# Performance work log

Hardware: AMD Instinct MI355X
Metric: run time of the kernel (lower is better)

## Reference

```python
import jax, jax.numpy as jnp
import numpy as np

N, D, H, T = 50000, 512, 512, 16
N_HOP = 1
NEG = -1e18


def setup_inputs() -> dict:
    key = jax.random.key(0)
    ks = jax.random.split(key, 16)
    s = 0.05  # param init scale
    inp = {
        "attn_mem": jax.random.normal(ks[0], (N, D), jnp.float32),
        "stop": jax.random.uniform(ks[1], (D,), jnp.float32, -0.01, 0.01),
        "init_h": jax.random.normal(ks[2], (H,), jnp.float32) * s,
        "init_c": jax.random.normal(ks[3], (H,), jnp.float32) * s,
        "init_i": jax.random.normal(ks[4], (D,), jnp.float32) * s,
        "attn_wm": jax.random.normal(ks[5], (D, H), jnp.float32) * s,
        "attn_wq": jax.random.normal(ks[6], (H, H), jnp.float32) * s,
        "attn_v": jax.random.normal(ks[7], (H,), jnp.float32) * s,
        "hop_wm": jax.random.normal(ks[8], (D, H), jnp.float32) * s,
        "hop_wq": jax.random.normal(ks[9], (H, H), jnp.float32) * s,
        "hop_v": jax.random.normal(ks[10], (H,), jnp.float32) * s,
        "w_ih": jax.random.normal(ks[11], (4 * H, D), jnp.float32) * s,
        "w_hh": jax.random.normal(ks[12], (4 * H, H), jnp.float32) * s,
        "b_ih": jax.random.normal(ks[13], (4 * H,), jnp.float32) * s,
        "b_hh": jax.random.normal(ks[14], (4 * H,), jnp.float32) * s,
        # precomputed gumbel noise -> categorical sampling via gumbel-max
        "gumbel": jax.random.gumbel(ks[15], (T, N + 1), jnp.float32),
    }
    return inp


def _attn_score(feat, q, v, w):
    # feat: [M, H], q: [H] -> unnormalized scores [M]
    return jnp.tanh(feat + q @ w) @ v


def reference(attn_mem, stop, init_h, init_c, init_i, attn_wm, attn_wq, attn_v,
              hop_wm, hop_wq, hop_v, w_ih, w_hh, b_ih, b_hh, gumbel):
    mem = jnp.concatenate([attn_mem, stop[None, :]], axis=0)  # [N+1, D]
    attn_feat = mem @ attn_wm                                  # [N+1, H]
    hop_feat = mem @ hop_wm                                    # [N+1, H]
    stop_idx = mem.shape[0] - 1

    def lstm_cell(x, h, c):
        gates = x @ w_ih.T + b_ih + h @ w_hh.T + b_hh          # [4H]
        i, f, g, o = jnp.split(gates, 4)
        i, f, o = jax.nn.sigmoid(i), jax.nn.sigmoid(f), jax.nn.sigmoid(o)
        c_new = f * c + i * jnp.tanh(g)
        return o * jnp.tanh(c_new), c_new

    def step(carry, g):
        h, c, x, sel, done = carry
        h, c = lstm_cell(x, h, c)
        q = h
        for _ in range(N_HOP):  # glimpse hops
            s = _attn_score(hop_feat, q, hop_v, hop_wq)
            q = jax.nn.softmax(s) @ hop_feat
        score = _attn_score(attn_feat, q, attn_v, attn_wq)     # [N+1]
        score = jnp.where(sel, NEG, score)                     # mask selected
        logp_all = jax.nn.log_softmax(score)
        out = jnp.argmax(score + g)                            # Categorical sample
        logp = jnp.where(done, 0.0, logp_all[out])
        out_rec = jnp.where(done, stop_idx, out)
        sel = jnp.where(done, sel, sel.at[out].set(True))
        new_done = done | (out == stop_idx)
        x = jnp.where(new_done, x, mem[out])
        return (h, c, x, sel, new_done), (out_rec.astype(jnp.int32), logp)

    carry0 = (init_h, init_c, init_i,
              jnp.zeros((mem.shape[0],), jnp.bool_), jnp.array(False))
    _, (outs, logps) = jax.lax.scan(step, carry0, gumbel)
    return outs, logps
```

## Files before the change

kernel.cpp:

```cpp
#include <hip/hip_runtime.h>
#include <math.h>

#define NITEMS 50000
#define NROWS 50001
#define NP 50176
#define DD 512
#define HH 512
#define TT 16
#define NEGV (-1e18f)
#define NGRP 784
#define NGC 196

typedef unsigned long long ull;
typedef unsigned short ushort;
typedef short short8 __attribute__((ext_vector_type(8)));
typedef float f32x4 __attribute__((ext_vector_type(4)));

#define AST(p, v) __hip_atomic_store((p), (v), __ATOMIC_RELAXED, __HIP_MEMORY_SCOPE_AGENT)
#define ALD(p) __hip_atomic_load((p), __ATOMIC_RELAXED, __HIP_MEMORY_SCOPE_AGENT)
#define AADD_REL(p) __hip_atomic_fetch_add((p), 1u, __ATOMIC_ACQ_REL, __HIP_MEMORY_SCOPE_AGENT)
#define FLAG_SET(p) __hip_atomic_store((p), 1u, __ATOMIC_RELEASE, __HIP_MEMORY_SCOPE_AGENT)
#define FLAG_GET(p) __hip_atomic_load((p), __ATOMIC_ACQUIRE, __HIP_MEMORY_SCOPE_AGENT)

__device__ __forceinline__ unsigned fkey(float f) {
  unsigned u = __float_as_uint(f);
  return (u & 0x80000000u) ? ~u : (u | 0x80000000u);
}
__device__ __forceinline__ float ftanh(float x) {
  float e = __builtin_amdgcn_exp2f(x * 2.885390081777927f);
  return 1.f - 2.f * __builtin_amdgcn_rcpf(e + 1.f);
}
__device__ __forceinline__ float fexp(float x) {
  return __builtin_amdgcn_exp2f(x * 1.4426950408889634f);
}
__device__ __forceinline__ ushort rne1(float a) {
  unsigned u = __float_as_uint(a);
  return (ushort)((u + 0x7fffu + ((u >> 16) & 1u)) >> 16);
}
__device__ __forceinline__ float bf2f(ushort h) { return __uint_as_float((unsigned)h << 16); }
__device__ __forceinline__ unsigned pack_bf16(float a, float b) {
  return (unsigned)rne1(a) | ((unsigned)rne1(b) << 16);
}
__device__ __forceinline__ float bflo(unsigned u) { return __uint_as_float(u << 16); }
__device__ __forceinline__ float bfhi(unsigned u) { return __uint_as_float(u & 0xffff0000u); }

__device__ __forceinline__ void gl_lds16(const void* g, void* l) {
#if __has_builtin(__builtin_amdgcn_global_load_lds)
  __builtin_amdgcn_global_load_lds((const __attribute__((address_space(1))) unsigned*)g,
                                   (__attribute__((address_space(3))) unsigned*)l, 16, 0, 0);
#else
  const int lane = threadIdx.x & 63;
  *(uint4*)((char*)l + lane * 16) = *(const uint4*)g;
#endif
}

#define MFMA(a, b, c) __builtin_amdgcn_mfma_f32_16x16x32_bf16(a, b, c, 0, 0, 0)

__global__ void k_convA(const float* __restrict__ A0, const float* __restrict__ stoprow,
                        ushort* __restrict__ Ahi, ushort* __restrict__ Alo) {
  const size_t t = (size_t)blockIdx.x * 256 + threadIdx.x;
  const size_t base = t * 8;
  const int row = (int)(base >> 9);
  float v[8];
  if (row < NITEMS) {
    const float4* p = (const float4*)(A0 + base);
    float4 x = p[0], y = p[1];
    v[0] = x.x; v[1] = x.y; v[2] = x.z; v[3] = x.w;
    v[4] = y.x; v[5] = y.y; v[6] = y.z; v[7] = y.w;
  } else if (row == NITEMS) {
    const float4* p = (const float4*)(stoprow + (base & 511));
    float4 x = p[0], y = p[1];
    v[0] = x.x; v[1] = x.y; v[2] = x.z; v[3] = x.w;
    v[4] = y.x; v[5] = y.y; v[6] = y.z; v[7] = y.w;
  } else {
#pragma unroll
    for (int j = 0; j < 8; ++j) v[j] = 0.f;
  }
  unsigned hw[4], lw[4];
#pragma unroll
  for (int j = 0; j < 4; ++j) {
    float a0 = v[2 * j], a1 = v[2 * j + 1];
    ushort h0 = rne1(a0), h1 = rne1(a1);
    hw[j] = (unsigned)h0 | ((unsigned)h1 << 16);
    lw[j] = pack_bf16(a0 - bf2f(h0), a1 - bf2f(h1));
  }
  *(uint4*)(Ahi + base) = make_uint4(hw[0], hw[1], hw[2], hw[3]);
  *(uint4*)(Alo + base) = make_uint4(lw[0], lw[1], lw[2], lw[3]);
}

__global__ void k_convBT(const float* __restrict__ W, ushort* __restrict__ WhiT,
                         ushort* __restrict__ WloT) {
  const int n = blockIdx.x;
  const int k0 = threadIdx.x * 2;
  float a0 = W[(size_t)k0 * 512 + n];
  float a1 = W[(size_t)(k0 + 1) * 512 + n];
  ushort h0 = rne1(a0), h1 = rne1(a1);
  *(unsigned*)(WhiT + (size_t)n * 512 + k0) = (unsigned)h0 | ((unsigned)h1 << 16);
  *(unsigned*)(WloT + (size_t)n * 512 + k0) = pack_bf16(a0 - bf2f(h0), a1 - bf2f(h1));
}

template <int TR>
__launch_bounds__(256, 2)
__global__ void k_mfma(const ushort* __restrict__ Ahi, const ushort* __restrict__ Alo,
                       const ushort* __restrict__ BhT, const ushort* __restrict__ BlT,
                       ushort* __restrict__ C) {
  __shared__ __align__(16) char lds[65536];
  char* sA0 = lds;
  char* sA1 = lds + 16384;
  char* sB0 = lds + 32768;
  char* sB1 = lds + 49152;
  const int tid = threadIdx.x;
  const int lane = tid & 63, w = tid >> 6;
  const int lid = blockIdx.y * 4 + blockIdx.x;
  const int xcd = lid & 7, pos = lid >> 3;
  const int orig = xcd * 196 + pos;
  const int m0 = (orig >> 2) * 128, n0 = (orig & 3) * 128;
  const int aR0 = (w & 1) * 64, bR0 = (w >> 1) * 64;

  f32x4 acc[4][4];
  const f32x4 z4 = {0.f, 0.f, 0.f, 0.f};
#pragma unroll
  for (int i = 0; i < 4; ++i)
#pragma unroll
    for (int j = 0; j < 4; ++j) acc[i][j] = z4;

#define STAGE_ALL(KT)                                                                     \
  {                                                                                       \
    _Pragma("unroll") for (int i = 0; i < 4; ++i) {                                       \
      const int row = i * 32 + (tid >> 3);                                                \
      const int kb = ((tid & 7) << 4) ^ ((row & 7) << 4);                                 \
      const int ldso = i * 4096 + (w << 10);                                              \
      gl_lds16((const char*)(Ahi + ((size_t)(m0 + row) << 9) + (KT)) + kb, sA0 + ldso);   \
      gl_lds16((const char*)(Alo + ((size_t)(m0 + row) << 9) + (KT)) + kb, sA1 + ldso);   \
      gl_lds16((const char*)(BhT + ((size_t)(n0 + row) << 9) + (KT)) + kb, sB0 + ldso);   \
      gl_lds16((const char*)(BlT + ((size_t)(n0 + row) << 9) + (KT)) + kb, sB1 + ldso);   \
    }                                                                                     \
  }

  STAGE_ALL(0)
  __syncthreads();
  for (int c = 0; c < 8; ++c) {
#pragma unroll
    for (int ks = 0; ks < 2; ++ks) {
      short8 ah[4], al[4], bh[4], bl[4];
      const int kbb = ks * 64 + ((lane >> 4) << 4);
#pragma unroll
      for (int f = 0; f < 4; ++f) {
        const int ra = aR0 + f * 16 + (lane & 15);
        const int oa = ra * 128 + (kbb ^ ((ra & 7) << 4));
        ah[f] = *(const short8*)(sA0 + oa);
        al[f] = *(const short8*)(sA1 + oa);
        const int rb = bR0 + f * 16 + (lane & 15);
        const int ob = rb * 128 + (kbb ^ ((rb & 7) << 4));
        bh[f] = *(const short8*)(sB0 + ob);
        bl[f] = *(const short8*)(sB1 + ob);
      }
#pragma unroll
      for (int mf = 0; mf < 4; ++mf)
#pragma unroll
        for (int nf = 0; nf < 4; ++nf) {
          acc[mf][nf] = MFMA(ah[mf], bh[nf], acc[mf][nf]);
          acc[mf][nf] = MFMA(ah[mf], bl[nf], acc[mf][nf]);
          acc[mf][nf] = MFMA(al[mf], bh[nf], acc[mf][nf]);
        }
    }
    if (c < 7) {
      __syncthreads();
      STAGE_ALL((c + 1) * 64)
      __syncthreads();
    }
  }
#undef STAGE_ALL

#pragma unroll
  for (int mf = 0; mf < 4; ++mf)
#pragma unroll
    for (int nf = 0; nf < 4; ++nf) {
      const f32x4 a = acc[mf][nf];
      const int n = n0 + bR0 + nf * 16 + (lane & 15);
      const int mb = m0 + aR0 + mf * 16 + ((lane >> 4) << 2);
      if (TR) {
        ushort* p = C + (size_t)n * NP + mb;
        *(uint2*)p = make_uint2(pack_bf16(a.x, a.y), pack_bf16(a.z, a.w));
      } else {
        C[(size_t)(mb + 0) * 512 + n] = rne1(a.x);
        C[(size_t)(mb + 1) * 512 + n] = rne1(a.y);
        C[(size_t)(mb + 2) * 512 + n] = rne1(a.z);
        C[(size_t)(mb + 3) * 512 + n] = rne1(a.w);
      }
    }
}

__global__ void k_zero(int* __restrict__ sel, unsigned* __restrict__ cnts) {
  int i = blockIdx.x * 256 + threadIdx.x;
  if (i < NROWS) sel[i] = 0;
  if (blockIdx.x == 0 && threadIdx.x < 80) cnts[threadIdx.x] = 0;
}

__launch_bounds__(256)
__global__ void k_A(const float* __restrict__ attn_mem, const float* __restrict__ stoprow,
                    const float* __restrict__ init_i, const float* __restrict__ init_h,
                    const float* __restrict__ init_c,
                    const float* __restrict__ w_ih, const float* __restrict__ w_hh,
                    const float* __restrict__ b_ih, const float* __restrict__ b_hh,
                    const float* __restrict__ hop_wq,
                    float* __restrict__ hv0, float* __restrict__ hv1,
                    float* __restrict__ cv0, float* __restrict__ cv1,
                    float* __restrict__ b1, const int* __restrict__ xrow_buf,
                    unsigned* __restrict__ cntA, unsigned* __restrict__ flagA, int t) {
  __shared__ float g4[4];
  __shared__ float hs[512];
  __shared__ float red2[256];
  __shared__ int sOld;
  const int b = blockIdx.x, tid = threadIdx.x, w = tid >> 6, lane = tid & 63;
  const int xrow = (t == 0) ? -1 : *xrow_buf;
  const float* xp = (xrow < 0) ? init_i
                               : ((xrow == NITEMS) ? stoprow : attn_mem + (size_t)xrow * DD);
  const float* hsrc = (t == 0) ? init_h : ((t & 1) ? hv0 : hv1);
  float* hdst = (t & 1) ? hv1 : hv0;
  const float* csrc = (t == 0) ? init_c : ((t & 1) ? cv0 : cv1);
  float* cdst = (t & 1) ? cv1 : cv0;

  const int r = w * 512 + b;
  const float4* x4 = (const float4*)xp;
  const float4* h4 = (const float4*)hsrc;
  const float4* wi = (const float4*)(w_ih + (size_t)r * DD);
  const float4* wh = (const float4*)(w_hh + (size_t)r * DD);
  float s = 0.f;
  float4 a, ww;
  a = x4[lane * 2];     ww = wi[lane * 2];     s += a.x * ww.x + a.y * ww.y + a.z * ww.z + a.w * ww.w;
  a = x4[lane * 2 + 1]; ww = wi[lane * 2 + 1]; s += a.x * ww.x + a.y * ww.y + a.z * ww.z + a.w * ww.w;
  a = h4[lane * 2];     ww = wh[lane * 2];     s += a.x * ww.x + a.y * ww.y + a.z * ww.z + a.w * ww.w;
  a = h4[lane * 2 + 1]; ww = wh[lane * 2 + 1]; s += a.x * ww.x + a.y * ww.y + a.z * ww.z + a.w * ww.w;
#pragma unroll
  for (int off = 32; off > 0; off >>= 1) s += __shfl_xor(s, off);
  if (lane == 0) g4[w] = s + b_ih[r] + b_hh[r];
  __syncthreads();
  if (tid == 0) {
    const float si = 1.f / (1.f + expf(-g4[0]));
    const float sf = 1.f / (1.f + expf(-g4[1]));
    const float so = 1.f / (1.f + expf(-g4[3]));
    const float cn = sf * csrc[b] + si * tanhf(g4[2]);
    cdst[b] = cn;
    AST(&hdst[b], so * tanhf(cn));
  }
  __syncthreads();
  if (tid == 0) {
    unsigned old = AADD_REL(cntA);
    if (old == 511u) { FLAG_SET(flagA); AST(cntA, 0u); }
    sOld = (int)old;
  }
  __syncthreads();
  const int old = sOld;
  if (old >= 496) {
    if (tid == 0 && old != 511) {
      while (FLAG_GET(flagA) == 0u) {}
    }
    __syncthreads();
    const int c0 = (old - 496) * 32;
    hs[tid] = ALD(&hdst[tid]);
    hs[tid + 256] = ALD(&hdst[tid + 256]);
    __syncthreads();
    const int col = c0 + (tid & 31), seg = tid >> 5;
    float acc = 0.f;
#pragma unroll 8
    for (int i = seg * 64; i < seg * 64 + 64; ++i)
      acc = fmaf(hs[i], hop_wq[(size_t)i * 512 + col], acc);
    red2[tid] = acc;
    __syncthreads();
    if (tid < 32) {
      float sm = 0.f;
#pragma unroll
      for (int g2 = 0; g2 < 8; ++g2) sm += red2[tid + 32 * g2];
      b1[c0 + tid] = sm;
    }
  }
}

__launch_bounds__(512)
__global__ void k_B1(const ushort* __restrict__ featT, const float* __restrict__ b1v,
                     const float* __restrict__ hv, float* __restrict__ e,
                     float* __restrict__ bZ1, float* __restrict__ Zt,
                     unsigned* __restrict__ cntB1) {
  __shared__ float spart[8][256];
  __shared__ float rz[512];
  __shared__ int isLast;
  const int tid = threadIdx.x, g = blockIdx.x;
  const int w = tid >> 6, lane = tid & 63;
  const int mb = g * 256 + lane * 4;
  const int h0 = w * 64;
  const ushort* fp = featT + (size_t)h0 * NP + mb;
  float a0 = 0.f, a1 = 0.f, a2 = 0.f, a3 = 0.f;
#pragma unroll 8
  for (int hh = 0; hh < 64; ++hh) {
    const uint2 u = *(const uint2*)fp;
    fp += NP;
    const float bb = b1v[h0 + hh], vv = hv[h0 + hh];
    a0 += ftanh(bflo(u.x) + bb) * vv;
    a1 += ftanh(bfhi(u.x) + bb) * vv;
    a2 += ftanh(bflo(u.y) + bb) * vv;
    a3 += ftanh(bfhi(u.y) + bb) * vv;
  }
  spart[w][lane * 4 + 0] = a0;
  spart[w][lane * 4 + 1] = a1;
  spart[w][lane * 4 + 2] = a2;
  spart[w][lane * 4 + 3] = a3;
  __syncthreads();
  if (w < 4) {
    const int idx = w * 64 + lane;
    const int m = g * 256 + idx;
    float s = 0.f;
#pragma unroll
    for (int w2 = 0; w2 < 8; ++w2) s += spart[w2][idx];
    float ev = (m < NROWS) ? fexp(s) : 0.f;
    e[m] = ev;
    float Z = ev;
#pragma unroll
    for (int off = 32; off > 0; off >>= 1) Z += __shfl_xor(Z, off);
    if (lane == 0) AST(&bZ1[g * 4 + w], Z);
  }
  __syncthreads();
  if (tid == 0) {
    unsigned old = AADD_REL(cntB1);
    isLast = (old == gridDim.x - 1);
    if (isLast) AST(cntB1, 0u);
  }
  __syncthreads();
  if (isLast) {
    float Zl = 0.f;
    for (int i = tid; i < NGRP; i += 512) Zl += ALD(&bZ1[i]);
    rz[tid] = Zl;
    __syncthreads();
    for (int s2 = 256; s2 > 0; s2 >>= 1) {
      if (tid < s2) rz[tid] += rz[tid + s2];
      __syncthreads();
    }
    if (tid == 0) *Zt = rz[0];
  }
}

__launch_bounds__(256)
__global__ void k_B2(const ushort* __restrict__ featT, const float* __restrict__ e,
                     const float* __restrict__ Zt, const float* __restrict__ attn_wq,
                     float* __restrict__ qn, float* __restrict__ b2,
                     unsigned* __restrict__ cntB2, unsigned* __restrict__ flagB2) {
  __shared__ float red[256];
  __shared__ int sOld;
  const int tid = threadIdx.x, h = blockIdx.x;
  const ushort* fr = featT + (size_t)h * NP;
  float acc = 0.f;
#pragma unroll 4
  for (int m0 = tid * 8; m0 < NP; m0 += 2048) {
    const uint4 F = *(const uint4*)(fr + m0);
    const float4 e0 = *(const float4*)(e + m0);
    const float4 e1 = *(const float4*)(e + m0 + 4);
    acc += bflo(F.x) * e0.x + bfhi(F.x) * e0.y + bflo(F.y) * e0.z + bfhi(F.y) * e0.w +
           bflo(F.z) * e1.x + bfhi(F.z) * e1.y + bflo(F.w) * e1.z + bfhi(F.w) * e1.w;
  }
  red[tid] = acc;
  __syncthreads();
  for (int s2 = 128; s2 > 0; s2 >>= 1) {
    if (tid < s2) red[tid] += red[tid + s2];
    __syncthreads();
  }
  if (tid == 0) AST(&qn[h], red[0] / (*Zt));
  __syncthreads();
  if (tid == 0) {
    unsigned old = AADD_REL(cntB2);
    if (old == 511u) { FLAG_SET(flagB2); AST(cntB2, 0u); }
    sOld = (int)old;
  }
  __syncthreads();
  const int old = sOld;
  if (old >= 504) {
    const int li = old - 504;
    if (tid == 0 && old != 511) {
      while (FLAG_GET(flagB2) == 0u) {}
    }
    __syncthreads();
    const int j = li * 64 + (tid & 63), is = tid >> 6;
    float a = 0.f;
#pragma unroll 8
    for (int i2 = is * 128; i2 < is * 128 + 128; ++i2)
      a = fmaf(ALD(&qn[i2]), attn_wq[(size_t)i2 * 512 + j], a);
    red[tid] = a;
    __syncthreads();
    if (tid < 64) b2[li * 64 + tid] = red[tid] + red[tid + 64] + red[tid + 128] + red[tid + 192];
  }
}

__launch_bounds__(512)
__global__ void k_C(const ushort* __restrict__ featT, const float* __restrict__ b2,
                    const float* __restrict__ av, int* __restrict__ sel,
                    const float* __restrict__ gum,
                    float* __restrict__ bZa, ull* __restrict__ bkey, float* __restrict__ bsc,
                    int* __restrict__ done_buf, int* __restrict__ xrow_buf,
                    float* __restrict__ outf, unsigned* __restrict__ cntC, int t) {
  __shared__ float spart[8][256];
  __shared__ float rz[512];
  __shared__ ull rk[512];
  __shared__ float rs[512];
  __shared__ int isLast;
  const int tid = threadIdx.x, g = blockIdx.x;
  const int w = tid >> 6, lane = tid & 63;
  const int mb = g * 256 + lane * 4;
  const int h0 = w * 64;
  const ushort* fp = featT + (size_t)h0 * NP + mb;
  float a0 = 0.f, a1 = 0.f, a2 = 0.f, a3 = 0.f;
#pragma unroll 8
  for (int hh = 0; hh < 64; ++hh) {
    const uint2 u = *(const uint2*)fp;
    fp += NP;
    const float bb = b2[h0 + hh], vv = av[h0 + hh];
    a0 += ftanh(bflo(u.x) + bb) * vv;
    a1 += ftanh(bfhi(u.x) + bb) * vv;
    a2 += ftanh(bflo(u.y) + bb) * vv;
    a3 += ftanh(bfhi(u.y) + bb) * vv;
  }
  spart[w][lane * 4 + 0] = a0;
  spart[w][lane * 4 + 1] = a1;
  spart[w][lane * 4 + 2] = a2;
  spart[w][lane * 4 + 3] = a3;
  __syncthreads();
  if (w < 4) {
    const int idx = w * 64 + lane;
    const int m = g * 256 + idx;
    float s = 0.f;
#pragma unroll
    for (int w2 = 0; w2 < 8; ++w2) s += spart[w2][idx];
    const bool valid = (m < NROWS);
    float Z, sv;
    ull key;
    if (valid) {
      const float se = sel[m] ? NEGV : s;
      sv = se;
      key = ((ull)fkey(se + gum[m]) << 32) | (unsigned)(NITEMS - m);
      Z = fexp(se);
    } else {
      key = 0;
      Z = 0.f;
      sv = 0.f;
    }
#pragma unroll
    for (int off = 32; off > 0; off >>= 1) {
      Z += __shfl_xor(Z, off);
      ull Ko = __shfl_xor(key, off);
      float so = __shfl_xor(sv, off);
      if (Ko > key) { key = Ko; sv = so; }
    }
    if (lane == 0) {
      AST(&bZa[g * 4 + w], Z);
      AST(&bkey[g * 4 + w], key);
      AST(&bsc[g * 4 + w], sv);
    }
  }
  __syncthreads();
  if (tid == 0) {
    unsigned old = AADD_REL(cntC);
    isLast = (old == gridDim.x - 1);
    if (isLast) AST(cntC, 0u);
  }
  __syncthreads();
  if (isLast) {
    float Zl = 0.f, Sl = 0.f;
    ull Kl = 0;
    for (int i = tid; i < NGRP; i += 512) {
      Zl += ALD(&bZa[i]);
      ull k = ALD(&bkey[i]);
      if (k > Kl) { Kl = k; Sl = ALD(&bsc[i]); }
    }
    rz[tid] = Zl;
    rk[tid] = Kl;
    rs[tid] = Sl;
    __syncthreads();
    for (int s2 = 256; s2 > 0; s2 >>= 1) {
      if (tid < s2) {
        rz[tid] += rz[tid + s2];
        if (rk[tid + s2] > rk[tid]) { rk[tid] = rk[tid + s2]; rs[tid] = rs[tid + s2]; }
      }
      __syncthreads();
    }
    if (tid == 0) {
      const float Z = rz[0];
      const ull K = rk[0];
      const int out = NITEMS - (int)(unsigned)(K & 0xffffffffull);
      const int d_in = (t == 0) ? 0 : *done_buf;
      const int xprev = (t == 0) ? -1 : *xrow_buf;
      const int nd = d_in | (out == NITEMS);
      outf[t] = (float)(d_in ? NITEMS : out);
      outf[TT + t] = d_in ? 0.f : (rs[0] - logf(Z));
      if (!d_in) sel[out] = 1;
      *done_buf = nd;
      *xrow_buf = nd ? xprev : out;
    }
  }
}

extern "C" void kernel_launch(void* const* d_in, const int* in_sizes, int n_in,
                              void* d_out, int out_size, void* d_ws, size_t ws_size,
                              hipStream_t stream) {
  const float* attn_mem = (const float*)d_in[0];
  const float* stoprow  = (const float*)d_in[1];
  const float* init_h   = (const float*)d_in[2];
  const float* init_c   = (const float*)d_in[3];
  const float* init_i   = (const float*)d_in[4];
  const float* attn_wm  = (const float*)d_in[5];
  const float* attn_wq  = (const float*)d_in[6];
  const float* attn_v   = (const float*)d_in[7];
  const float* hop_wm   = (const float*)d_in[8];
  const float* hop_wq   = (const float*)d_in[9];
  const float* hop_v    = (const float*)d_in[10];
  const float* w_ih     = (const float*)d_in[11];
  const float* w_hh     = (const float*)d_in[12];
  const float* b_ih     = (const float*)d_in[13];
  const float* b_hh     = (const float*)d_in[14];
  const float* gumbel   = (const float*)d_in[15];

  float* ws = (float*)d_ws;
  size_t fo = 0;
  const size_t FB = (size_t)NP * 512 / 2;
  ushort* hop_featT  = (ushort*)(ws + fo); fo += FB;
  ushort* attn_featT = (ushort*)(ws + fo); fo += FB;
  ushort* Ahi = (ushort*)(ws + fo); fo += FB;
  ushort* Alo = (ushort*)(ws + fo); fo += FB;
  ushort* WhiT_a = (ushort*)(ws + fo); fo += 131072;
  ushort* WloT_a = (ushort*)(ws + fo); fo += 131072;
  ushort* WhiT_h = (ushort*)(ws + fo); fo += 131072;
  ushort* WloT_h = (ushort*)(ws + fo); fo += 131072;
  int* sel   = (int*)(ws + fo); fo += NP;
  float* e   = ws + fo; fo += NP;
  float* bZ1 = ws + fo; fo += 1024;
  float* bZa = ws + fo; fo += 1024;
  float* bsc = ws + fo; fo += 1024;
  ull* bkey  = (ull*)(ws + fo); fo += 2048;
  float* hv0 = ws + fo; fo += HH;
  float* hv1 = ws + fo; fo += HH;
  float* cv0 = ws + fo; fo += HH;
  float* cv1 = ws + fo; fo += HH;
  float* b1  = ws + fo; fo += HH;
  float* b2  = ws + fo; fo += HH;
  float* qn  = ws + fo; fo += HH;
  float* Ztp = ws + fo; fo += 2;
  unsigned* cnts = (unsigned*)(ws + fo); fo += 80;
  int* done_buf = (int*)(ws + fo); fo += 2;
  int* xrow_buf = (int*)(ws + fo); fo += 2;
  if (fo * sizeof(float) > ws_size) return;

  float* outf = (float*)d_out;

  k_zero<<<NP / 256, 256, 0, stream>>>(sel, cnts);
  k_convA<<<(NP * 512 / 8) / 256, 256, 0, stream>>>(attn_mem, stoprow, Ahi, Alo);
  k_convBT<<<512, 256, 0, stream>>>(attn_wm, WhiT_a, WloT_a);
  k_convBT<<<512, 256, 0, stream>>>(hop_wm, WhiT_h, WloT_h);

  dim3 ggrid(4, NP / 128);
  k_mfma<1><<<ggrid, 256, 0, stream>>>(Ahi, Alo, WhiT_a, WloT_a, attn_featT);
  k_mfma<1><<<ggrid, 256, 0, stream>>>(Ahi, Alo, WhiT_h, WloT_h, hop_featT);

  for (int t = 0; t < TT; ++t) {
    k_A<<<512, 256, 0, stream>>>(attn_mem, stoprow, init_i, init_h, init_c,
                                 w_ih, w_hh, b_ih, b_hh, hop_wq,
                                 hv0, hv1, cv0, cv1, b1, xrow_buf,
                                 cnts + 0, cnts + 16 + t, t);
    k_B1<<<NGC, 512, 0, stream>>>(hop_featT, b1, hop_v, e, bZ1, Ztp, cnts + 1);
    k_B2<<<512, 256, 0, stream>>>(hop_featT, e, Ztp, attn_wq, qn, b2,
                                  cnts + 3, cnts + 32 + t);
    k_C<<<NGC, 512, 0, stream>>>(attn_featT, b2, attn_v, sel,
                                 gumbel + (size_t)t * NROWS, bZa, bkey, bsc,
                                 done_buf, xrow_buf, outf, cnts + 2, t);
  }
}
```

Before: 1.624 ms.

## Fuse per-step kernels into one grid-synchronized step kernel

```diff
diff --git a/kernel.cpp b/kernel.cpp
--- a/kernel.cpp
+++ b/kernel.cpp
@@ -9,7 +9,7 @@
 #define TT 16
 #define NEGV (-1e18f)
 #define NGRP 784
-#define NGC 196
+#define NSB 512
 
 typedef unsigned long long ull;
 typedef unsigned short ushort;
@@ -99,7 +99,6 @@
   *(unsigned*)(WloT + (size_t)n * 512 + k0) = pack_bf16(a0 - bf2f(h0), a1 - bf2f(h1));
 }
 
-template <int TR>
 __launch_bounds__(256, 2)
 __global__ void k_mfma(const ushort* __restrict__ Ahi, const ushort* __restrict__ Alo,
                        const ushort* __restrict__ BhT, const ushort* __restrict__ BlT,
@@ -179,22 +178,15 @@
       const f32x4 a = acc[mf][nf];
       const int n = n0 + bR0 + nf * 16 + (lane & 15);
       const int mb = m0 + aR0 + mf * 16 + ((lane >> 4) << 2);
-      if (TR) {
-        ushort* p = C + (size_t)n * NP + mb;
-        *(uint2*)p = make_uint2(pack_bf16(a.x, a.y), pack_bf16(a.z, a.w));
-      } else {
-        C[(size_t)(mb + 0) * 512 + n] = rne1(a.x);
-        C[(size_t)(mb + 1) * 512 + n] = rne1(a.y);
-        C[(size_t)(mb + 2) * 512 + n] = rne1(a.z);
-        C[(size_t)(mb + 3) * 512 + n] = rne1(a.w);
-      }
+      ushort* p = C + (size_t)n * NP + mb;
+      *(uint2*)p = make_uint2(pack_bf16(a.x, a.y), pack_bf16(a.z, a.w));
     }
 }
 
 __global__ void k_zero(int* __restrict__ sel, unsigned* __restrict__ cnts) {
   int i = blockIdx.x * 256 + threadIdx.x;
   if (i < NROWS) sel[i] = 0;
-  if (blockIdx.x == 0 && threadIdx.x < 80) cnts[threadIdx.x] = 0;
+  if (blockIdx.x == 0 && threadIdx.x < 128) cnts[threadIdx.x] = 0;
 }
 
 __launch_bounds__(256)
@@ -213,7 +205,7 @@
   __shared__ float red2[256];
   __shared__ int sOld;
   const int b = blockIdx.x, tid = threadIdx.x, w = tid >> 6, lane = tid & 63;
-  const int xrow = (t == 0) ? -1 : *xrow_buf;
+  const int xrow = (t == 0) ? -1 : ALD((int*)xrow_buf);
   const float* xp = (xrow < 0) ? init_i
                                : ((xrow == NITEMS) ? stoprow : attn_mem + (size_t)xrow * DD);
   const float* hsrc = (t == 0) ? init_h : ((t & 1) ? hv0 : hv1);
@@ -254,7 +246,7 @@
   const int old = sOld;
   if (old >= 496) {
     if (tid == 0 && old != 511) {
-      while (FLAG_GET(flagA) == 0u) {}
+      while (FLAG_GET(flagA) == 0u) __builtin_amdgcn_s_sleep(2);
     }
     __syncthreads();
     const int c0 = (old - 496) * 32;
@@ -277,221 +269,316 @@
   }
 }
 
-__launch_bounds__(512)
-__global__ void k_B1(const ushort* __restrict__ featT, const float* __restrict__ b1v,
-                     const float* __restrict__ hv, float* __restrict__ e,
-                     float* __restrict__ bZ1, float* __restrict__ Zt,
-                     unsigned* __restrict__ cntB1) {
-  __shared__ float spart[8][256];
-  __shared__ float rz[512];
-  __shared__ int isLast;
-  const int tid = threadIdx.x, g = blockIdx.x;
+struct SP {
+  const ushort *hopT, *attnT;
+  const float *b1v, *hop_v, *attn_wq, *attn_v, *gumbel;
+  float *e, *bZ1, *qn, *b2, *bZa, *bsc;
+  ull* bkey;
+  int* sel;
+  int *done_buf, *xrow_buf;
+  float* outf;
+  const float *attn_mem, *stoprow, *init_i, *init_h, *init_c;
+  const float *w_ih, *w_hh, *b_ih, *b_hh, *hop_wq;
+  float *hv0, *hv1, *cv0, *cv1, *b1out;
+  unsigned* cnts;
+  int t;
+};
+
+union SMu {
+  struct { float spart[4][128]; float bias[512]; float vv[512]; } sw;
+  struct { float red[256]; } r;
+  struct { float rz[256]; ull rk[256]; float rs[256]; } fin;
+  struct { float g4[4]; float hs[512]; float red2[256]; } pa;
+};
+
+__launch_bounds__(256)
+__global__ void k_step(SP p) {
+  __shared__ SMu sm;
+  __shared__ int sOld;
+  const int tid = threadIdx.x, b = blockIdx.x;
   const int w = tid >> 6, lane = tid & 63;
-  const int mb = g * 256 + lane * 4;
-  const int h0 = w * 64;
-  const ushort* fp = featT + (size_t)h0 * NP + mb;
-  float a0 = 0.f, a1 = 0.f, a2 = 0.f, a3 = 0.f;
+  const int t = p.t;
+  unsigned* c1 = p.cnts + 0;
+  unsigned* c2 = p.cnts + 1;
+  unsigned* c2b = p.cnts + 2;
+  unsigned* c3 = p.cnts + 3;
+  unsigned* cA = p.cnts + 4;
+  unsigned* f1 = p.cnts + 16 + t;
+  unsigned* f2a = p.cnts + 32 + t;
+  unsigned* f2 = p.cnts + 48 + t;
+  unsigned* fF = p.cnts + 64 + t;
+  unsigned* fA = p.cnts + 80 + t;
+
+  for (int i = tid; i < 512; i += 256) {
+    sm.sw.bias[i] = p.b1v[i];
+    sm.sw.vv[i] = p.hop_v[i];
+  }
+  __syncthreads();
+  if (b < 392) {
+    const int mb = b * 128 + lane * 2;
+    const int h0 = w * 128;
+    const ushort* fp = p.hopT + (size_t)h0 * NP + mb;
+    float a0 = 0.f, a1 = 0.f;
 #pragma unroll 8
-  for (int hh = 0; hh < 64; ++hh) {
-    const uint2 u = *(const uint2*)fp;
-    fp += NP;
-    const float bb = b1v[h0 + hh], vv = hv[h0 + hh];
-    a0 += ftanh(bflo(u.x) + bb) * vv;
-    a1 += ftanh(bfhi(u.x) + bb) * vv;
-    a2 += ftanh(bflo(u.y) + bb) * vv;
-    a3 += ftanh(bfhi(u.y) + bb) * vv;
-  }
-  spart[w][lane * 4 + 0] = a0;
-  spart[w][lane * 4 + 1] = a1;
-  spart[w][lane * 4 + 2] = a2;
-  spart[w][lane * 4 + 3] = a3;
-  __syncthreads();
-  if (w < 4) {
-    const int idx = w * 64 + lane;
-    const int m = g * 256 + idx;
-    float s = 0.f;
-#pragma unroll
-    for (int w2 = 0; w2 < 8; ++w2) s += spart[w2][idx];
-    float ev = (m < NROWS) ? fexp(s) : 0.f;
-    e[m] = ev;
-    float Z = ev;
-#pragma unroll
-    for (int off = 32; off > 0; off >>= 1) Z += __shfl_xor(Z, off);
-    if (lane == 0) AST(&bZ1[g * 4 + w], Z);
+    for (int hh = 0; hh < 128; ++hh) {
+      const unsigned u = *(const unsigned*)fp;
+      fp += NP;
+      const float bb = sm.sw.bias[h0 + hh], vv = sm.sw.vv[h0 + hh];
+      a0 += ftanh(bflo(u) + bb) * vv;
+      a1 += ftanh(bfhi(u) + bb) * vv;
+    }
+    sm.sw.spart[w][lane * 2] = a0;
+    sm.sw.spart[w][lane * 2 + 1] = a1;
+    __syncthreads();
+    if (w < 2) {
+      const int idx = w * 64 + lane;
+      const int m = b * 128 + idx;
+      float s = sm.sw.spart[0][idx] + sm.sw.spart[1][idx] + sm.sw.spart[2][idx] +
+                sm.sw.spart[3][idx];
+      float ev = (m < NROWS) ? fexp(s) : 0.f;
+      p.e[m] = ev;
+      float Z = ev;
+#pragma unroll
+      for (int off = 32; off > 0; off >>= 1) Z += __shfl_xor(Z, off);
+      if (lane == 0) AST(&p.bZ1[b * 2 + w], Z);
+    }
   }
   __syncthreads();
   if (tid == 0) {
-    unsigned old = AADD_REL(cntB1);
-    isLast = (old == gridDim.x - 1);
-    if (isLast) AST(cntB1, 0u);
-  }
-  __syncthreads();
-  if (isLast) {
-    float Zl = 0.f;
-    for (int i = tid; i < NGRP; i += 512) Zl += ALD(&bZ1[i]);
-    rz[tid] = Zl;
-    __syncthreads();
-    for (int s2 = 256; s2 > 0; s2 >>= 1) {
-      if (tid < s2) rz[tid] += rz[tid + s2];
-      __syncthreads();
-    }
-    if (tid == 0) *Zt = rz[0];
-  }
-}
-
-__launch_bounds__(256)
-__global__ void k_B2(const ushort* __restrict__ featT, const float* __restrict__ e,
-                     const float* __restrict__ Zt, const float* __restrict__ attn_wq,
-                     float* __restrict__ qn, float* __restrict__ b2,
-                     unsigned* __restrict__ cntB2, unsigned* __restrict__ flagB2) {
-  __shared__ float red[256];
-  __shared__ int sOld;
-  const int tid = threadIdx.x, h = blockIdx.x;
-  const ushort* fr = featT + (size_t)h * NP;
-  float acc = 0.f;
+    unsigned old = AADD_REL(c1);
+    if (old == NSB - 1u) { FLAG_SET(f1); AST(c1, 0u); }
+    else { while (FLAG_GET(f1) == 0u) __builtin_amdgcn_s_sleep(2); }
+  }
+  __syncthreads();
+
+  {
+    const ushort* fr = p.hopT + (size_t)b * NP;
+    float acc = 0.f;
 #pragma unroll 4
-  for (int m0 = tid * 8; m0 < NP; m0 += 2048) {
-    const uint4 F = *(const uint4*)(fr + m0);
-    const float4 e0 = *(const float4*)(e + m0);
-    const float4 e1 = *(const float4*)(e + m0 + 4);
-    acc += bflo(F.x) * e0.x + bfhi(F.x) * e0.y + bflo(F.y) * e0.z + bfhi(F.y) * e0.w +
-           bflo(F.z) * e1.x + bfhi(F.z) * e1.y + bflo(F.w) * e1.z + bfhi(F.w) * e1.w;
-  }
-  red[tid] = acc;
-  __syncthreads();
-  for (int s2 = 128; s2 > 0; s2 >>= 1) {
-    if (tid < s2) red[tid] += red[tid + s2];
-    __syncthreads();
-  }
-  if (tid == 0) AST(&qn[h], red[0] / (*Zt));
+    for (int m0 = tid * 8; m0 < NP; m0 += 2048) {
+      const uint4 F = *(const uint4*)(fr + m0);
+      const float4 e0 = *(const float4*)(p.e + m0);
+      const float4 e1 = *(const float4*)(p.e + m0 + 4);
+      acc += bflo(F.x) * e0.x + bfhi(F.x) * e0.y + bflo(F.y) * e0.z + bfhi(F.y) * e0.w +
+             bflo(F.z) * e1.x + bfhi(F.z) * e1.y + bflo(F.w) * e1.z + bfhi(F.w) * e1.w;
+    }
+    sm.r.red[tid] = acc;
+    __syncthreads();
+    for (int s2 = 128; s2 > 0; s2 >>= 1) {
+      if (tid < s2) sm.r.red[tid] += sm.r.red[tid + s2];
+      __syncthreads();
+    }
+    if (tid == 0) AST(&p.qn[b], sm.r.red[0]);
+  }
   __syncthreads();
   if (tid == 0) {
-    unsigned old = AADD_REL(cntB2);
-    if (old == 511u) { FLAG_SET(flagB2); AST(cntB2, 0u); }
+    unsigned old = AADD_REL(c2);
     sOld = (int)old;
-  }
-  __syncthreads();
-  const int old = sOld;
-  if (old >= 504) {
-    const int li = old - 504;
-    if (tid == 0 && old != 511) {
-      while (FLAG_GET(flagB2) == 0u) {}
-    }
-    __syncthreads();
+    if (old == NSB - 1u) { FLAG_SET(f2a); AST(c2, 0u); }
+    else if (old >= NSB - 8u) {
+      while (FLAG_GET(f2a) == 0u) __builtin_amdgcn_s_sleep(2);
+    }
+  }
+  __syncthreads();
+  const int o2 = sOld;
+  if (o2 >= NSB - 8) {
+    float zl = 0.f;
+    for (int i = tid; i < NGRP; i += 256) zl += ALD(&p.bZ1[i]);
+    sm.r.red[tid] = zl;
+    __syncthreads();
+    for (int s2 = 128; s2 > 0; s2 >>= 1) {
+      if (tid < s2) sm.r.red[tid] += sm.r.red[tid + s2];
+      __syncthreads();
+    }
+    const float Zt = sm.r.red[0];
+    __syncthreads();
+    const int li = o2 - (NSB - 8);
     const int j = li * 64 + (tid & 63), is = tid >> 6;
     float a = 0.f;
 #pragma unroll 8
     for (int i2 = is * 128; i2 < is * 128 + 128; ++i2)
-      a = fmaf(ALD(&qn[i2]), attn_wq[(size_t)i2 * 512 + j], a);
-    red[tid] = a;
-    __syncthreads();
-    if (tid < 64) b2[li * 64 + tid] = red[tid] + red[tid + 64] + red[tid + 128] + red[tid + 192];
-  }
-}
-
-__launch_bounds__(512)
-__global__ void k_C(const ushort* __restrict__ featT, const float* __restrict__ b2,
-                    const float* __restrict__ av, int* __restrict__ sel,
-                    const float* __restrict__ gum,
-                    float* __restrict__ bZa, ull* __restrict__ bkey, float* __restrict__ bsc,
-                    int* __restrict__ done_buf, int* __restrict__ xrow_buf,
-                    float* __restrict__ outf, unsigned* __restrict__ cntC, int t) {
-  __shared__ float spart[8][256];
-  __shared__ float rz[512];
-  __shared__ ull rk[512];
-  __shared__ float rs[512];
-  __shared__ int isLast;
-  const int tid = threadIdx.x, g = blockIdx.x;
-  const int w = tid >> 6, lane = tid & 63;
-  const int mb = g * 256 + lane * 4;
-  const int h0 = w * 64;
-  const ushort* fp = featT + (size_t)h0 * NP + mb;
-  float a0 = 0.f, a1 = 0.f, a2 = 0.f, a3 = 0.f;
+      a = fmaf(ALD(&p.qn[i2]), p.attn_wq[(size_t)i2 * 512 + j], a);
+    sm.r.red[tid] = a;
+    __syncthreads();
+    if (tid < 64)
+      AST(&p.b2[li * 64 + tid],
+          (sm.r.red[tid] + sm.r.red[tid + 64] + sm.r.red[tid + 128] + sm.r.red[tid + 192]) / Zt);
+    __syncthreads();
+    if (tid == 0) {
+      unsigned ob = AADD_REL(c2b);
+      if (ob == 7u) { FLAG_SET(f2); AST(c2b, 0u); }
+    }
+  }
+  if (tid == 0) {
+    while (FLAG_GET(f2) == 0u) __builtin_amdgcn_s_sleep(2);
+  }
+  __syncthreads();
+
+  for (int i = tid; i < 512; i += 256) {
+    sm.sw.bias[i] = ALD(&p.b2[i]);
+    sm.sw.vv[i] = p.attn_v[i];
+  }
+  __syncthreads();
+  if (b < 392) {
+    const int mb = b * 128 + lane * 2;
+    const int h0 = w * 128;
+    const ushort* fp = p.attnT + (size_t)h0 * NP + mb;
+    float a0 = 0.f, a1 = 0.f;
 #pragma unroll 8
-  for (int hh = 0; hh < 64; ++hh) {
-    const uint2 u = *(const uint2*)fp;
-    fp += NP;
-    const float bb = b2[h0 + hh], vv = av[h0 + hh];
-    a0 += ftanh(bflo(u.x) + bb) * vv;
-    a1 += ftanh(bfhi(u.x) + bb) * vv;
-    a2 += ftanh(bflo(u.y) + bb) * vv;
-    a3 += ftanh(bfhi(u.y) + bb) * vv;
-  }
-  spart[w][lane * 4 + 0] = a0;
-  spart[w][lane * 4 + 1] = a1;
-  spart[w][lane * 4 + 2] = a2;
-  spart[w][lane * 4 + 3] = a3;
-  __syncthreads();
-  if (w < 4) {
-    const int idx = w * 64 + lane;
-    const int m = g * 256 + idx;
-    float s = 0.f;
-#pragma unroll
-    for (int w2 = 0; w2 < 8; ++w2) s += spart[w2][idx];
-    const bool valid = (m < NROWS);
-    float Z, sv;
-    ull key;
-    if (valid) {
-      const float se = sel[m] ? NEGV : s;
-      sv = se;
-      key = ((ull)fkey(se + gum[m]) << 32) | (unsigned)(NITEMS - m);
-      Z = fexp(se);
-    } else {
-      key = 0;
-      Z = 0.f;
-      sv = 0.f;
-    }
-#pragma unroll
-    for (int off = 32; off > 0; off >>= 1) {
-      Z += __shfl_xor(Z, off);
-      ull Ko = __shfl_xor(key, off);
-      float so = __shfl_xor(sv, off);
-      if (Ko > key) { key = Ko; sv = so; }
-    }
-    if (lane == 0) {
-      AST(&bZa[g * 4 + w], Z);
-      AST(&bkey[g * 4 + w], key);
-      AST(&bsc[g * 4 + w], sv);
+    for (int hh = 0; hh < 128; ++hh) {
+      const unsigned u = *(const unsigned*)fp;
+      fp += NP;
+      const float bb = sm.sw.bias[h0 + hh], vv = sm.sw.vv[h0 + hh];
+      a0 += ftanh(bflo(u) + bb) * vv;
+      a1 += ftanh(bfhi(u) + bb) * vv;
+    }
+    sm.sw.spart[w][lane * 2] = a0;
+    sm.sw.spart[w][lane * 2 + 1] = a1;
+    __syncthreads();
+    if (w < 2) {
+      const int idx = w * 64 + lane;
+      const int m = b * 128 + idx;
+      float s = sm.sw.spart[0][idx] + sm.sw.spart[1][idx] + sm.sw.spart[2][idx] +
+                sm.sw.spart[3][idx];
+      const bool valid = (m < NROWS);
+      float Z, sv;
+      ull key;
+      if (valid) {
+        const float se = p.sel[m] ? NEGV : s;
+        sv = se;
+        key = ((ull)fkey(se + p.gumbel[m]) << 32) | (unsigned)(NITEMS - m);
+        Z = fexp(se);
+      } else {
+        key = 0;
+        Z = 0.f;
+        sv = 0.f;
+      }
+#pragma unroll
+      for (int off = 32; off > 0; off >>= 1) {
+        Z += __shfl_xor(Z, off);
+        ull Ko = __shfl_xor(key, off);
+        float so = __shfl_xor(sv, off);
+        if (Ko > key) { key = Ko; sv = so; }
+      }
+      if (lane == 0) {
+        AST(&p.bZa[b * 2 + w], Z);
+        AST(&p.bkey[b * 2 + w], key);
+        AST(&p.bsc[b * 2 + w], sv);
+      }
     }
   }
   __syncthreads();
   if (tid == 0) {
-    unsigned old = AADD_REL(cntC);
-    isLast = (old == gridDim.x - 1);
-    if (isLast) AST(cntC, 0u);
-  }
-  __syncthreads();
-  if (isLast) {
+    unsigned old = AADD_REL(c3);
+    sOld = (int)old;
+    if (old == NSB - 1u) AST(c3, 0u);
+  }
+  __syncthreads();
+  if (sOld == NSB - 1) {
     float Zl = 0.f, Sl = 0.f;
     ull Kl = 0;
-    for (int i = tid; i < NGRP; i += 512) {
-      Zl += ALD(&bZa[i]);
-      ull k = ALD(&bkey[i]);
-      if (k > Kl) { Kl = k; Sl = ALD(&bsc[i]); }
-    }
-    rz[tid] = Zl;
-    rk[tid] = Kl;
-    rs[tid] = Sl;
-    __syncthreads();
-    for (int s2 = 256; s2 > 0; s2 >>= 1) {
+    for (int i = tid; i < NGRP; i += 256) {
+      Zl += ALD(&p.bZa[i]);
+      ull k = ALD(&p.bkey[i]);
+      if (k > Kl) { Kl = k; Sl = ALD(&p.bsc[i]); }
+    }
+    sm.fin.rz[tid] = Zl;
+    sm.fin.rk[tid] = Kl;
+    sm.fin.rs[tid] = Sl;
+    __syncthreads();
+    for (int s2 = 128; s2 > 0; s2 >>= 1) {
       if (tid < s2) {
-        rz[tid] += rz[tid + s2];
-        if (rk[tid + s2] > rk[tid]) { rk[tid] = rk[tid + s2]; rs[tid] = rs[tid + s2]; }
+        sm.fin.rz[tid] += sm.fin.rz[tid + s2];
+        if (sm.fin.rk[tid + s2] > sm.fin.rk[tid]) {
+          sm.fin.rk[tid] = sm.fin.rk[tid + s2];
+          sm.fin.rs[tid] = sm.fin.rs[tid + s2];
+        }
       }
       __syncthreads();
     }
     if (tid == 0) {
-      const float Z = rz[0];
-      const ull K = rk[0];
+      const float Z = sm.fin.rz[0];
+      const ull K = sm.fin.rk[0];
       const int out = NITEMS - (int)(unsigned)(K & 0xffffffffull);
-      const int d_in = (t == 0) ? 0 : *done_buf;
-      const int xprev = (t == 0) ? -1 : *xrow_buf;
+      const int d_in = (t == 0) ? 0 : ALD(p.done_buf);
+      const int xprev = (t == 0) ? -1 : ALD(p.xrow_buf);
       const int nd = d_in | (out == NITEMS);
-      outf[t] = (float)(d_in ? NITEMS : out);
-      outf[TT + t] = d_in ? 0.f : (rs[0] - logf(Z));
-      if (!d_in) sel[out] = 1;
-      *done_buf = nd;
-      *xrow_buf = nd ? xprev : out;
+      p.outf[t] = (float)(d_in ? NITEMS : out);
+      p.outf[TT + t] = d_in ? 0.f : (sm.fin.rs[0] - logf(Z));
+      if (!d_in) p.sel[out] = 1;
+      AST(p.done_buf, nd);
+      AST(p.xrow_buf, nd ? xprev : out);
+      FLAG_SET(fF);
+    }
+  }
+  if (tid == 0) {
+    while (FLAG_GET(fF) == 0u) __builtin_amdgcn_s_sleep(2);
+  }
+  __syncthreads();
+
+  {
+    const int tA = t + 1;
+    const int xrow = ALD(p.xrow_buf);
+    const float* xp = (xrow < 0) ? p.init_i
+                                 : ((xrow == NITEMS) ? p.stoprow : p.attn_mem + (size_t)xrow * DD);
+    const float* hsrc = (tA & 1) ? p.hv0 : p.hv1;
+    float* hdst = (tA & 1) ? p.hv1 : p.hv0;
+    const float* csrc = (tA & 1) ? p.cv0 : p.cv1;
+    float* cdst = (tA & 1) ? p.cv1 : p.cv0;
+
+    const int r = w * 512 + b;
+    const float4* x4 = (const float4*)xp;
+    const float4* h4 = (const float4*)hsrc;
+    const float4* wi = (const float4*)(p.w_ih + (size_t)r * DD);
+    const float4* wh = (const float4*)(p.w_hh + (size_t)r * DD);
+    float s = 0.f;
+    float4 a, ww;
+    a = x4[lane * 2];     ww = wi[lane * 2];     s += a.x * ww.x + a.y * ww.y + a.z * ww.z + a.w * ww.w;
+    a = x4[lane * 2 + 1]; ww = wi[lane * 2 + 1]; s += a.x * ww.x + a.y * ww.y + a.z * ww.z + a.w * ww.w;
+    a = h4[lane * 2];     ww = wh[lane * 2];     s += a.x * ww.x + a.y * ww.y + a.z * ww.z + a.w * ww.w;
+    a = h4[lane * 2 + 1]; ww = wh[lane * 2 + 1]; s += a.x * ww.x + a.y * ww.y + a.z * ww.z + a.w * ww.w;
+#pragma unroll
+    for (int off = 32; off > 0; off >>= 1) s += __shfl_xor(s, off);
+    if (lane == 0) sm.pa.g4[w] = s + p.b_ih[r] + p.b_hh[r];
+    __syncthreads();
+    if (tid == 0) {
+      const float si = 1.f / (1.f + expf(-sm.pa.g4[0]));
+      const float sf = 1.f / (1.f + expf(-sm.pa.g4[1]));
+      const float so = 1.f / (1.f + expf(-sm.pa.g4[3]));
+      const float cn = sf * csrc[b] + si * tanhf(sm.pa.g4[2]);
+      cdst[b] = cn;
+      AST(&hdst[b], so * tanhf(cn));
+    }
+    __syncthreads();
+    if (tid == 0) {
+      unsigned old = AADD_REL(cA);
+      if (old == NSB - 1u) { FLAG_SET(fA); AST(cA, 0u); }
+      sOld = (int)old;
+    }
+    __syncthreads();
+    const int old = sOld;
+    if (old >= NSB - 16) {
+      if (tid == 0 && old != NSB - 1) {
+        while (FLAG_GET(fA) == 0u) __builtin_amdgcn_s_sleep(2);
+      }
+      __syncthreads();
+      const int c0 = (old - (NSB - 16)) * 32;
+      sm.pa.hs[tid] = ALD(&hdst[tid]);
+      sm.pa.hs[tid + 256] = ALD(&hdst[tid + 256]);
+      __syncthreads();
+      const int col = c0 + (tid & 31), seg = tid >> 5;
+      float acc = 0.f;
+#pragma unroll 8
+      for (int i = seg * 64; i < seg * 64 + 64; ++i)
+        acc = fmaf(sm.pa.hs[i], p.hop_wq[(size_t)i * 512 + col], acc);
+      sm.pa.red2[tid] = acc;
+      __syncthreads();
+      if (tid < 32) {
+        float s2 = 0.f;
+#pragma unroll
+        for (int g2 = 0; g2 < 8; ++g2) s2 += sm.pa.red2[tid + 32 * g2];
+        p.b1out[c0 + tid] = s2;
+      }
     }
   }
 }
@@ -540,8 +627,7 @@
   float* b1  = ws + fo; fo += HH;
   float* b2  = ws + fo; fo += HH;
   float* qn  = ws + fo; fo += HH;
-  float* Ztp = ws + fo; fo += 2;
-  unsigned* cnts = (unsigned*)(ws + fo); fo += 80;
+  unsigned* cnts = (unsigned*)(ws + fo); fo += 128;
   int* done_buf = (int*)(ws + fo); fo += 2;
   int* xrow_buf = (int*)(ws + fo); fo += 2;
   if (fo * sizeof(float) > ws_size) return;
@@ -554,19 +640,29 @@
   k_convBT<<<512, 256, 0, stream>>>(hop_wm, WhiT_h, WloT_h);
 
   dim3 ggrid(4, NP / 128);
-  k_mfma<1><<<ggrid, 256, 0, stream>>>(Ahi, Alo, WhiT_a, WloT_a, attn_featT);
-  k_mfma<1><<<ggrid, 256, 0, stream>>>(Ahi, Alo, WhiT_h, WloT_h, hop_featT);
+  k_mfma<<<ggrid, 256, 0, stream>>>(Ahi, Alo, WhiT_a, WloT_a, attn_featT);
+  k_mfma<<<ggrid, 256, 0, stream>>>(Ahi, Alo, WhiT_h, WloT_h, hop_featT);
+
+  k_A<<<NSB, 256, 0, stream>>>(attn_mem, stoprow, init_i, init_h, init_c,
+                               w_ih, w_hh, b_ih, b_hh, hop_wq,
+                               hv0, hv1, cv0, cv1, b1, xrow_buf,
+                               cnts + 5, cnts + 96, 0);
+
+  SP p;
+  p.hopT = hop_featT; p.attnT = attn_featT;
+  p.b1v = b1; p.hop_v = hop_v; p.attn_wq = attn_wq; p.attn_v = attn_v;
+  p.e = e; p.bZ1 = bZ1; p.qn = qn; p.b2 = b2;
+  p.bZa = bZa; p.bsc = bsc; p.bkey = bkey;
+  p.sel = sel; p.done_buf = done_buf; p.xrow_buf = xrow_buf; p.outf = outf;
+  p.attn_mem = attn_mem; p.stoprow = stoprow;
+  p.init_i = init_i; p.init_h = init_h; p.init_c = init_c;
+  p.w_ih = w_ih; p.w_hh = w_hh; p.b_ih = b_ih; p.b_hh = b_hh; p.hop_wq = hop_wq;
+  p.hv0 = hv0; p.hv1 = hv1; p.cv0 = cv0; p.cv1 = cv1; p.b1out = b1;
+  p.cnts = cnts;
 
   for (int t = 0; t < TT; ++t) {
-    k_A<<<512, 256, 0, stream>>>(attn_mem, stoprow, init_i, init_h, init_c,
-                                 w_ih, w_hh, b_ih, b_hh, hop_wq,
-                                 hv0, hv1, cv0, cv1, b1, xrow_buf,
-                                 cnts + 0, cnts + 16 + t, t);
-    k_B1<<<NGC, 512, 0, stream>>>(hop_featT, b1, hop_v, e, bZ1, Ztp, cnts + 1);
-    k_B2<<<512, 256, 0, stream>>>(hop_featT, e, Ztp, attn_wq, qn, b2,
-                                  cnts + 3, cnts + 32 + t);
-    k_C<<<NGC, 512, 0, stream>>>(attn_featT, b2, attn_v, sel,
-                                 gumbel + (size_t)t * NROWS, bZa, bkey, bsc,
-                                 done_buf, xrow_buf, outf, cnts + 2, t);
-  }
-}
+    p.gumbel = gumbel + (size_t)t * NROWS;
+    p.t = t;
+    k_step<<<NSB, 256, 0, stream>>>(p);
+  }
+}
```

Result: slower. 4.509 ms (+177.7%).
